# Kernel optimization log

Measured on AMD Instinct MI355X. Metric: run time of the kernel, lower is better.

## Reference

```python
import jax, jax.numpy as jnp
import numpy as np

B, H, W, C = 4, 64, 64, 256
D = C // 8  # q/k projection dim


def setup_inputs() -> dict:
    key = jax.random.key(0)
    ks = jax.random.split(key, 5)
    scale = lambda fan_in: 1.0 / np.sqrt(fan_in)
    return {
        "x": jax.random.normal(ks[0], (B, H, W, C), dtype=jnp.float32),
        "wq": jax.random.normal(ks[1], (C, D), dtype=jnp.float32) * scale(C),
        "bq": jnp.zeros((D,), dtype=jnp.float32),
        "wk": jax.random.normal(ks[2], (C, D), dtype=jnp.float32) * scale(C),
        "bk": jnp.zeros((D,), dtype=jnp.float32),
        "wv": jax.random.normal(ks[3], (C, C), dtype=jnp.float32) * scale(C),
        "bv": jnp.zeros((C,), dtype=jnp.float32),
        "wo": jax.random.normal(ks[4], (C, C), dtype=jnp.float32) * scale(C),
        "bo": jnp.zeros((C,), dtype=jnp.float32),
    }


def reference(x, wq, bq, wk, bk, wv, bv, wo, bo):
    b, h, w, c = x.shape
    n = h * w
    xt = x.reshape(b, n, c)  # 1x1 conv == per-pixel linear over channels
    q = xt @ wq + bq                      # [b, n, d]
    k = xt @ wk + bk                      # [b, n, d]
    v = xt @ wv + bv                      # [b, n, c]
    scores = jnp.einsum("bnd,bmd->bnm", q, k) / jnp.sqrt(jnp.float32(k.shape[-1]))
    attn = jax.nn.softmax(scores, axis=-1)  # [b, n, n]
    attended = jnp.einsum("bnm,bmc->bnc", attn, v)  # [b, n, c]
    out = attended @ wo + bo
    return x + out.reshape(b, h, w, c)
```

## Files before the change

### kernel.cpp

```cpp
#include <hip/hip_runtime.h>
#include <math.h>

#define B_   4
#define N_   4096
#define C_   256
#define D_   32

typedef __attribute__((ext_vector_type(8))) short short8;
typedef __attribute__((ext_vector_type(4))) float f32x4;
typedef __attribute__((ext_vector_type(4))) unsigned short us4;

__device__ __forceinline__ unsigned short f2bf(float f) {
    unsigned int u = __float_as_uint(f);
    u = (u + 0x7FFFu + ((u >> 16) & 1u)) >> 16;
    return (unsigned short)u;
}
__device__ __forceinline__ unsigned short p2bf(float f) {
    return (unsigned short)((__float_as_uint(f) + 0x8000u) >> 16);
}
__device__ __forceinline__ float bf2f(unsigned short h) {
    return __uint_as_float(((unsigned int)h) << 16);
}

__device__ __forceinline__ void dma16(const unsigned short* g, unsigned short* l) {
    __builtin_amdgcn_global_load_lds(
        (const __attribute__((address_space(1))) unsigned int*)(uintptr_t)(g),
        (__attribute__((address_space(3))) unsigned int*)(unsigned int)(uintptr_t)(l),
        16, 0, 0);
}

__global__ __launch_bounds__(256) void prep_w_kernel(const float* __restrict__ wq,
                                                     const float* __restrict__ wk,
                                                     const float* __restrict__ wv,
                                                     const float* __restrict__ wo,
                                                     unsigned short* __restrict__ wqkvT,
                                                     unsigned short* __restrict__ woT) {
    int idx = blockIdx.x * 256 + threadIdx.x;
    if (idx < 320 * 256) {
        int n = idx >> 8, c = idx & 255;
        float v = (n < 32) ? wq[c * 32 + n]
                : (n < 64) ? wk[c * 32 + (n - 32)]
                           : wv[c * 256 + (n - 64)];
        wqkvT[idx] = f2bf(v);
    } else {
        int j = idx - 320 * 256;
        int n = j >> 8, c = j & 255;
        woT[j] = f2bf(wo[c * 256 + n]);
    }
}

__global__ __launch_bounds__(256) void qkv_gemm_kernel(const float* __restrict__ x,
        const unsigned short* __restrict__ wqkvT,
        const float* __restrict__ bq, const float* __restrict__ bk, const float* __restrict__ bv,
        unsigned short* __restrict__ qb, unsigned short* __restrict__ kb,
        unsigned short* __restrict__ vT) {
    const int tid = threadIdx.x;
    const int wave = tid >> 6, lane = tid & 63;
    const int quad = lane >> 4, li = lane & 15;
    const int rows0 = blockIdx.x * 32;
    const float kS = 0.17677669529663687f * 1.4426950408889634f;

    __shared__ __align__(16) unsigned short xs[32 * 264];

#pragma unroll
    for (int i = 0; i < 8; ++i) {
        int flat = i * 256 + tid;
        int row = flat >> 6, c4 = flat & 63;
        float4 f = *(const float4*)(x + (size_t)(rows0 + row) * 256 + c4 * 4);
        us4 o = { f2bf(f.x), f2bf(f.y), f2bf(f.z), f2bf(f.w) };
        *(us4*)&xs[row * 264 + c4 * 4] = o;
    }
    __syncthreads();

    const int rowt = wave & 1;
    const int nt0 = (wave >> 1) * 10;
    const int r0 = rows0 + rowt * 16;

    short8 A[8];
#pragma unroll
    for (int kc = 0; kc < 8; ++kc)
        A[kc] = *(const short8*)&xs[(rowt * 16 + li) * 264 + kc * 32 + quad * 8];

#pragma unroll
    for (int j = 0; j < 10; ++j) {
        const int nt = nt0 + j;
        f32x4 acc = {0.f, 0.f, 0.f, 0.f};
#pragma unroll
        for (int kc = 0; kc < 8; ++kc) {
            short8 Bf = *(const short8*)(wqkvT + (size_t)(nt * 16 + li) * 256 + kc * 32 + quad * 8);
            acc = __builtin_amdgcn_mfma_f32_16x16x32_bf16(A[kc], Bf, acc, 0, 0, 0);
        }
        int n = nt * 16 + li;
        float bias = (nt < 2) ? bq[n] : (nt < 4) ? bk[n - 32] : bv[n - 64];
        if (nt < 4) {
            unsigned short* dst = (nt < 2) ? qb : kb;
            float scl = (nt < 2) ? kS : 1.0f;
            int d = (nt < 2) ? n : (n - 32);
#pragma unroll
            for (int jj = 0; jj < 4; ++jj)
                dst[(size_t)(r0 + quad * 4 + jj) * 32 + d] = f2bf((acc[jj] + bias) * scl);
        } else {
            int c = n - 64;
            int p = r0 + quad * 4;
            int b = p >> 12, ni = p & 4095;
            us4 hv = { f2bf(acc[0] + bias), f2bf(acc[1] + bias),
                       f2bf(acc[2] + bias), f2bf(acc[3] + bias) };
            *(us4*)(vT + ((size_t)(b * 256 + c) * 4096 + ni)) = hv;
        }
    }
}

__global__ __launch_bounds__(256, 2) void attn_partial_kernel(
        const unsigned short* __restrict__ qb, const unsigned short* __restrict__ kb,
        const unsigned short* __restrict__ vT,
        unsigned short* __restrict__ Obf, float* __restrict__ ml) {
    const int tid = threadIdx.x;
    const int wave = tid >> 6, lane = tid & 63;
    const int quad = lane >> 4, li = lane & 15;
    const int by = blockIdx.y, sg = blockIdx.z;
    const int pw = blockIdx.x * 128 + wave * 32;
    const int key0 = sg * 1024;

    __shared__ __align__(16) unsigned short smem[21504];
    unsigned short* v0 = smem;
    unsigned short* v1 = smem + 8192;
    unsigned short* pw_ = smem + 16384 + wave * 1280;

    short8 a_q[2];
#pragma unroll
    for (int qf = 0; qf < 2; ++qf)
        a_q[qf] = *(const short8*)(qb + (size_t)(by * N_ + pw + qf * 16 + li) * 32 + quad * 8);

    const int o8 = lane >> 3, s8 = lane & 7;
    const int sp = s8 ^ o8;
    const int chl = sp >> 2, chk = sp & 3;
    auto stage = [&](int kt, unsigned short* buf) {
#pragma unroll
        for (int h = 0; h < 4; ++h) {
            int ch = ((h * 32 + wave * 8 + o8) << 1) + chl;
            const unsigned short* g = vT + (size_t)(by * 256 + ch) * 4096
                                        + key0 + kt * 32 + chk * 8;
            dma16(g, buf + (h * 256 + wave * 64) * 8);
        }
    };

    stage(0, v0);

    const f32x4 Z = {0.f, 0.f, 0.f, 0.f};
    f32x4 O[2][16];
#pragma unroll
    for (int qf = 0; qf < 2; ++qf)
#pragma unroll
        for (int ct = 0; ct < 16; ++ct) O[qf][ct] = Z;
    f32x4 lsum[2] = {Z, Z};
    short8 ones;
#pragma unroll
    for (int j = 0; j < 8; ++j) ones[j] = (short)0x3F80;

    short8 kf0, kf1;
    {
        const unsigned short* krow = kb + (size_t)(by * N_ + key0) * 32;
        kf0 = *(const short8*)(krow + li * 32 + quad * 8);
        kf1 = *(const short8*)(krow + (16 + li) * 32 + quad * 8);
    }

    const int voff = (li >> 1) * 64 + ((((li & 1) * 4 + quad) ^ ((li >> 1) & 7)) * 8);

    unsigned short* vc = v0;
    unsigned short* vn = v1;
#pragma unroll 1
    for (int kt = 0; kt < 32; ++kt) {
        __builtin_amdgcn_s_waitcnt(0x0f70);
        __syncthreads();

        short8 kn0 = kf0, kn1 = kf1;
        if (kt < 31) {
            stage(kt + 1, vn);
            const unsigned short* krow = kb + (size_t)(by * N_ + key0 + (kt + 1) * 32) * 32;
            kn0 = *(const short8*)(krow + li * 32 + quad * 8);
            kn1 = *(const short8*)(krow + (16 + li) * 32 + quad * 8);
        }

#pragma unroll
        for (int qf = 0; qf < 2; ++qf) {
            f32x4 s0 = __builtin_amdgcn_mfma_f32_16x16x32_bf16(a_q[qf], kf0, Z, 0, 0, 0);
            f32x4 s1 = __builtin_amdgcn_mfma_f32_16x16x32_bf16(a_q[qf], kf1, Z, 0, 0, 0);
#pragma unroll
            for (int r = 0; r < 4; ++r) {
                float p0 = __builtin_amdgcn_exp2f(s0[r]);
                float p1 = __builtin_amdgcn_exp2f(s1[r]);
                pw_[(qf * 16 + quad * 4 + r) * 40 + li]      = p2bf(p0);
                pw_[(qf * 16 + quad * 4 + r) * 40 + 16 + li] = p2bf(p1);
            }
        }

        short8 ap0 = *(const short8*)(pw_ + li * 40 + quad * 8);
        short8 ap1 = *(const short8*)(pw_ + (16 + li) * 40 + quad * 8);
        lsum[0] = __builtin_amdgcn_mfma_f32_16x16x32_bf16(ap0, ones, lsum[0], 0, 0, 0);
        lsum[1] = __builtin_amdgcn_mfma_f32_16x16x32_bf16(ap1, ones, lsum[1], 0, 0, 0);
#pragma unroll
        for (int ct = 0; ct < 16; ++ct) {
            short8 bv8 = *(const short8*)(vc + ct * 512 + voff);
            O[0][ct] = __builtin_amdgcn_mfma_f32_16x16x32_bf16(ap0, bv8, O[0][ct], 0, 0, 0);
            O[1][ct] = __builtin_amdgcn_mfma_f32_16x16x32_bf16(ap1, bv8, O[1][ct], 0, 0, 0);
        }

        kf0 = kn0; kf1 = kn1;
        unsigned short* t = vc; vc = vn; vn = t;
    }

    __syncthreads();
    unsigned short* att = smem + wave * 4224;
    const int srow = lane & 15, scc = (lane >> 4) * 64;
#pragma unroll
    for (int qf = 0; qf < 2; ++qf) {
#pragma unroll
        for (int ct = 0; ct < 16; ++ct)
#pragma unroll
            for (int r = 0; r < 4; ++r)
                att[(quad * 4 + r) * 264 + ct * 16 + li] = f2bf(O[qf][ct][r]);
        const int pbase = by * N_ + pw + qf * 16;
        unsigned short* dst = Obf + ((size_t)(pbase + srow) * 4 + sg) * 256 + scc;
#pragma unroll
        for (int h = 0; h < 8; ++h)
            *(short8*)(dst + h * 8) = *(const short8*)(att + srow * 264 + scc + h * 8);
        if (li == 0) {
#pragma unroll
            for (int r = 0; r < 4; ++r) {
                int pp = pbase + quad * 4 + r;
                ml[pp * 4 + sg] = lsum[qf][r];
            }
        }
    }
}

__global__ __launch_bounds__(256) void merge_proj_kernel(
        const unsigned short* __restrict__ Obf, const float* __restrict__ ml,
        const unsigned short* __restrict__ woT, const float* __restrict__ x,
        const float* __restrict__ bo, float* __restrict__ out) {
    const int tid = threadIdx.x;
    const int px = blockIdx.x * 16;
    __shared__ __align__(16) unsigned short att[16 * 264];

    {
        const int row = tid >> 4, chc = tid & 15;
        const int p = px + row;
        float lt = ml[p * 4] + ml[p * 4 + 1] + ml[p * 4 + 2] + ml[p * 4 + 3];
        float inv = 1.0f / lt;
        float acc[16];
#pragma unroll
        for (int i = 0; i < 16; ++i) acc[i] = 0.f;
#pragma unroll
        for (int s = 0; s < 4; ++s) {
            const unsigned short* src = Obf + (size_t)(p * 4 + s) * 256 + chc * 16;
            short8 v0 = *(const short8*)(src);
            short8 v1 = *(const short8*)(src + 8);
#pragma unroll
            for (int jj = 0; jj < 8; ++jj) {
                acc[jj]     += bf2f((unsigned short)v0[jj]);
                acc[8 + jj] += bf2f((unsigned short)v1[jj]);
            }
        }
        short8 o0, o1;
#pragma unroll
        for (int jj = 0; jj < 8; ++jj) {
            o0[jj] = (short)f2bf(acc[jj] * inv);
            o1[jj] = (short)f2bf(acc[8 + jj] * inv);
        }
        *(short8*)&att[row * 264 + chc * 16]     = o0;
        *(short8*)&att[row * 264 + chc * 16 + 8] = o1;
    }
    __syncthreads();

    const int wave = tid >> 6, lane = tid & 63;
    const int quad = lane >> 4, li = lane & 15;
    short8 bfr[8];
#pragma unroll
    for (int kc = 0; kc < 8; ++kc)
        bfr[kc] = *(const short8*)&att[li * 264 + kc * 32 + quad * 8];
#pragma unroll
    for (int mt = 0; mt < 4; ++mt) {
        const int mtg = wave * 4 + mt;
        f32x4 acc = {0.f, 0.f, 0.f, 0.f};
#pragma unroll
        for (int kc = 0; kc < 8; ++kc) {
            short8 aw = *(const short8*)(woT + (size_t)(mtg * 16 + li) * 256 + kc * 32 + quad * 8);
            acc = __builtin_amdgcn_mfma_f32_16x16x32_bf16(aw, bfr[kc], acc, 0, 0, 0);
        }
        const int pg = px + li;
        const float4 xv  = *(const float4*)(x  + (size_t)pg * 256 + mtg * 16 + quad * 4);
        const float4 bv4 = *(const float4*)(bo + mtg * 16 + quad * 4);
        float4 o4;
        o4.x = acc[0] + xv.x + bv4.x;
        o4.y = acc[1] + xv.y + bv4.y;
        o4.z = acc[2] + xv.z + bv4.z;
        o4.w = acc[3] + xv.w + bv4.w;
        *(float4*)(out + (size_t)pg * 256 + mtg * 16 + quad * 4) = o4;
    }
}

extern "C" void kernel_launch(void* const* d_in, const int* in_sizes, int n_in,
                              void* d_out, int out_size, void* d_ws, size_t ws_size,
                              hipStream_t stream) {
    const float* x  = (const float*)d_in[0];
    const float* wq = (const float*)d_in[1];
    const float* bq = (const float*)d_in[2];
    const float* wk = (const float*)d_in[3];
    const float* bk = (const float*)d_in[4];
    const float* wv = (const float*)d_in[5];
    const float* bv = (const float*)d_in[6];
    const float* wo = (const float*)d_in[7];
    const float* bo = (const float*)d_in[8];
    float* out = (float*)d_out;

    char* ws = (char*)d_ws;
    unsigned short* wqkvT = (unsigned short*)(ws);
    unsigned short* woT   = (unsigned short*)(ws +   163840);
    unsigned short* qb    = (unsigned short*)(ws +   294912);
    unsigned short* kb    = (unsigned short*)(ws +  1343488);
    unsigned short* vT    = (unsigned short*)(ws +  2392064);
    unsigned short* Obf   = (unsigned short*)(ws + 10780672);
    float*          ml    = (float*)         (ws + 44335104);

    hipLaunchKernelGGL(prep_w_kernel,      dim3(576),       dim3(256), 0, stream, wq, wk, wv, wo, wqkvT, woT);
    hipLaunchKernelGGL(qkv_gemm_kernel,    dim3(512),       dim3(256), 0, stream, x, wqkvT, bq, bk, bv, qb, kb, vT);
    hipLaunchKernelGGL(attn_partial_kernel,dim3(32, 4, 4),  dim3(256), 0, stream, qb, kb, vT, Obf, ml);
    hipLaunchKernelGGL(merge_proj_kernel,  dim3(1024),      dim3(256), 0, stream, Obf, ml, woT, x, bo, out);
}
```

Measured before the change: 177.5 us.

## Restructure attention partial kernel to transposed score tiles with register-resident P

The attention inner loop now computes transposed score tiles (K·Q^T), so the exponentiated probabilities land directly in the register layout needed as the B operand of a 16x16x16 bf16 MFMA. This removes the per-iteration LDS round-trip for P. Row sums are now accumulated in scalar registers and reduced with shuffles instead of an extra MFMA against a ones vector. Work is retiled so each wave handles 64 queries by 128 channels with 64-key steps, which doubles the V staging buffer and halves the loop trip count. The cost is higher register pressure, a larger shared-memory footprint that may reduce occupancy, and a different swizzled layout for the output write.

Measured after the change: 262.3 us. 1.48x slower.

```diff
diff --git a/kernel.cpp b/kernel.cpp
--- a/kernel.cpp
+++ b/kernel.cpp
@@ -7,16 +7,16 @@
 #define D_   32
 
 typedef __attribute__((ext_vector_type(8))) short short8;
+typedef __attribute__((ext_vector_type(4))) short short4v;
 typedef __attribute__((ext_vector_type(4))) float f32x4;
 typedef __attribute__((ext_vector_type(4))) unsigned short us4;
+typedef __attribute__((ext_vector_type(2))) int i32x2;
+typedef __attribute__((ext_vector_type(4))) int i32x4;
 
 __device__ __forceinline__ unsigned short f2bf(float f) {
     unsigned int u = __float_as_uint(f);
     u = (u + 0x7FFFu + ((u >> 16) & 1u)) >> 16;
     return (unsigned short)u;
-}
-__device__ __forceinline__ unsigned short p2bf(float f) {
-    return (unsigned short)((__float_as_uint(f) + 0x8000u) >> 16);
 }
 __device__ __forceinline__ float bf2f(unsigned short h) {
     return __uint_as_float(((unsigned int)h) << 16);
@@ -28,6 +28,13 @@
         (__attribute__((address_space(3))) unsigned int*)(unsigned int)(uintptr_t)(l),
         16, 0, 0);
 }
+
+#if __has_builtin(__builtin_amdgcn_mfma_f32_16x16x16bf16_1k)
+#define MFMA16(acc, a, b) acc = __builtin_amdgcn_mfma_f32_16x16x16bf16_1k(a, b, acc, 0, 0, 0)
+#else
+#define MFMA16(acc, a, b) \
+    asm("s_nop 1\n\tv_mfma_f32_16x16x16_bf16 %0, %1, %2, %0" : "+v"(acc) : "v"(a), "v"(b))
+#endif
 
 __global__ __launch_bounds__(256) void prep_w_kernel(const float* __restrict__ wq,
                                                      const float* __restrict__ wk,
@@ -117,120 +124,136 @@
     const int tid = threadIdx.x;
     const int wave = tid >> 6, lane = tid & 63;
     const int quad = lane >> 4, li = lane & 15;
-    const int by = blockIdx.y, sg = blockIdx.z;
-    const int pw = blockIdx.x * 128 + wave * 32;
-    const int key0 = sg * 1024;
-
-    __shared__ __align__(16) unsigned short smem[21504];
+    const int by = blockIdx.y, seg = blockIdx.z;
+    const int qh = wave >> 1, chh = wave & 1;
+    const int qw = blockIdx.x * 128 + qh * 64;
+    const int key0 = seg * 1024;
+
+    __shared__ __align__(16) unsigned short smem[32768];
     unsigned short* v0 = smem;
-    unsigned short* v1 = smem + 8192;
-    unsigned short* pw_ = smem + 16384 + wave * 1280;
-
-    short8 a_q[2];
-#pragma unroll
-    for (int qf = 0; qf < 2; ++qf)
-        a_q[qf] = *(const short8*)(qb + (size_t)(by * N_ + pw + qf * 16 + li) * 32 + quad * 8);
-
-    const int o8 = lane >> 3, s8 = lane & 7;
-    const int sp = s8 ^ o8;
-    const int chl = sp >> 2, chk = sp & 3;
+    unsigned short* v1 = smem + 16384;
+
+    short8 a_q[4];
+#pragma unroll
+    for (int qf = 0; qf < 4; ++qf)
+        a_q[qf] = *(const short8*)(qb + (size_t)(by * N_ + qw + qf * 16 + li) * 32 + quad * 8);
+
+    const int sch = tid >> 3;
+    const int sgi = (tid & 7) ^ (sch & 7);
+    const unsigned short* vsrc0 = vT + (size_t)(by * 256 + sch) * 4096 + key0 + sgi * 8;
+    const int ldss = wave * 512;
     auto stage = [&](int kt, unsigned short* buf) {
 #pragma unroll
-        for (int h = 0; h < 4; ++h) {
-            int ch = ((h * 32 + wave * 8 + o8) << 1) + chl;
-            const unsigned short* g = vT + (size_t)(by * 256 + ch) * 4096
-                                        + key0 + kt * 32 + chk * 8;
-            dma16(g, buf + (h * 256 + wave * 64) * 8);
-        }
+        for (int h = 0; h < 8; ++h)
+            dma16(vsrc0 + kt * 64 + (size_t)h * 32 * 4096, buf + h * 2048 + ldss);
     };
-
     stage(0, v0);
 
     const f32x4 Z = {0.f, 0.f, 0.f, 0.f};
-    f32x4 O[2][16];
-#pragma unroll
-    for (int qf = 0; qf < 2; ++qf)
-#pragma unroll
-        for (int ct = 0; ct < 16; ++ct) O[qf][ct] = Z;
-    f32x4 lsum[2] = {Z, Z};
-    short8 ones;
-#pragma unroll
-    for (int j = 0; j < 8; ++j) ones[j] = (short)0x3F80;
-
-    short8 kf0, kf1;
-    {
-        const unsigned short* krow = kb + (size_t)(by * N_ + key0) * 32;
-        kf0 = *(const short8*)(krow + li * 32 + quad * 8);
-        kf1 = *(const short8*)(krow + (16 + li) * 32 + quad * 8);
-    }
-
-    const int voff = (li >> 1) * 64 + ((((li & 1) * 4 + quad) ^ ((li >> 1) & 7)) * 8);
+    f32x4 acc[8][4];
+#pragma unroll
+    for (int ct = 0; ct < 8; ++ct)
+#pragma unroll
+        for (int qf = 0; qf < 4; ++qf) acc[ct][qf] = Z;
+    float ps[4] = {0.f, 0.f, 0.f, 0.f};
+
+    short8 kf[4];
+#pragma unroll
+    for (int kk = 0; kk < 4; ++kk)
+        kf[kk] = *(const short8*)(kb + (size_t)(by * N_ + key0 + kk * 16 + li) * 32 + quad * 8);
+
+    const int w0 = (quad >> 1) ^ (li & 7);
+    const int vbl = (chh * 128 + li) * 64 + (quad & 1) * 4;
 
     unsigned short* vc = v0;
     unsigned short* vn = v1;
 #pragma unroll 1
-    for (int kt = 0; kt < 32; ++kt) {
+    for (int kt = 0; kt < 16; ++kt) {
         __builtin_amdgcn_s_waitcnt(0x0f70);
         __syncthreads();
 
-        short8 kn0 = kf0, kn1 = kf1;
-        if (kt < 31) {
+        short8 kn[4];
+        if (kt < 15) {
             stage(kt + 1, vn);
-            const unsigned short* krow = kb + (size_t)(by * N_ + key0 + (kt + 1) * 32) * 32;
-            kn0 = *(const short8*)(krow + li * 32 + quad * 8);
-            kn1 = *(const short8*)(krow + (16 + li) * 32 + quad * 8);
-        }
-
-#pragma unroll
-        for (int qf = 0; qf < 2; ++qf) {
-            f32x4 s0 = __builtin_amdgcn_mfma_f32_16x16x32_bf16(a_q[qf], kf0, Z, 0, 0, 0);
-            f32x4 s1 = __builtin_amdgcn_mfma_f32_16x16x32_bf16(a_q[qf], kf1, Z, 0, 0, 0);
-#pragma unroll
-            for (int r = 0; r < 4; ++r) {
-                float p0 = __builtin_amdgcn_exp2f(s0[r]);
-                float p1 = __builtin_amdgcn_exp2f(s1[r]);
-                pw_[(qf * 16 + quad * 4 + r) * 40 + li]      = p2bf(p0);
-                pw_[(qf * 16 + quad * 4 + r) * 40 + 16 + li] = p2bf(p1);
+            const unsigned short* krow = kb + (size_t)(by * N_ + key0 + (kt + 1) * 64) * 32;
+#pragma unroll
+            for (int kk = 0; kk < 4; ++kk)
+                kn[kk] = *(const short8*)(krow + (kk * 16 + li) * 32 + quad * 8);
+        } else {
+#pragma unroll
+            for (int kk = 0; kk < 4; ++kk) kn[kk] = kf[kk];
+        }
+
+#pragma unroll
+        for (int kk = 0; kk < 4; ++kk) {
+            short4v pb[4];
+#pragma unroll
+            for (int qf = 0; qf < 4; ++qf) {
+                f32x4 st = __builtin_amdgcn_mfma_f32_16x16x32_bf16(kf[kk], a_q[qf], Z, 0, 0, 0);
+                float p0 = __builtin_amdgcn_exp2f(st[0]);
+                float p1 = __builtin_amdgcn_exp2f(st[1]);
+                float p2 = __builtin_amdgcn_exp2f(st[2]);
+                float p3 = __builtin_amdgcn_exp2f(st[3]);
+                ps[qf] += (p0 + p1) + (p2 + p3);
+                unsigned u0 = __float_as_uint(p0) + 0x8000u;
+                unsigned u1 = __float_as_uint(p1) + 0x8000u;
+                unsigned u2 = __float_as_uint(p2) + 0x8000u;
+                unsigned u3 = __float_as_uint(p3) + 0x8000u;
+                i32x2 t;
+                t[0] = (int)((u0 >> 16) | (u1 & 0xFFFF0000u));
+                t[1] = (int)((u2 >> 16) | (u3 & 0xFFFF0000u));
+                pb[qf] = __builtin_bit_cast(short4v, t);
             }
-        }
-
-        short8 ap0 = *(const short8*)(pw_ + li * 40 + quad * 8);
-        short8 ap1 = *(const short8*)(pw_ + (16 + li) * 40 + quad * 8);
-        lsum[0] = __builtin_amdgcn_mfma_f32_16x16x32_bf16(ap0, ones, lsum[0], 0, 0, 0);
-        lsum[1] = __builtin_amdgcn_mfma_f32_16x16x32_bf16(ap1, ones, lsum[1], 0, 0, 0);
-#pragma unroll
-        for (int ct = 0; ct < 16; ++ct) {
-            short8 bv8 = *(const short8*)(vc + ct * 512 + voff);
-            O[0][ct] = __builtin_amdgcn_mfma_f32_16x16x32_bf16(ap0, bv8, O[0][ct], 0, 0, 0);
-            O[1][ct] = __builtin_amdgcn_mfma_f32_16x16x32_bf16(ap1, bv8, O[1][ct], 0, 0, 0);
-        }
-
-        kf0 = kn0; kf1 = kn1;
+            const int go = ((kk * 2) ^ w0) * 8;
+#pragma unroll
+            for (int ct = 0; ct < 8; ++ct) {
+                short4v av = *(const short4v*)(vc + vbl + ct * 1024 + go);
+                MFMA16(acc[ct][0], av, pb[0]);
+                MFMA16(acc[ct][1], av, pb[1]);
+                MFMA16(acc[ct][2], av, pb[2]);
+                MFMA16(acc[ct][3], av, pb[3]);
+            }
+        }
+#pragma unroll
+        for (int kk = 0; kk < 4; ++kk) kf[kk] = kn[kk];
         unsigned short* t = vc; vc = vn; vn = t;
     }
 
     __syncthreads();
-    unsigned short* att = smem + wave * 4224;
-    const int srow = lane & 15, scc = (lane >> 4) * 64;
-#pragma unroll
-    for (int qf = 0; qf < 2; ++qf) {
-#pragma unroll
-        for (int ct = 0; ct < 16; ++ct)
-#pragma unroll
-            for (int r = 0; r < 4; ++r)
-                att[(quad * 4 + r) * 264 + ct * 16 + li] = f2bf(O[qf][ct][r]);
-        const int pbase = by * N_ + pw + qf * 16;
-        unsigned short* dst = Obf + ((size_t)(pbase + srow) * 4 + sg) * 256 + scc;
-#pragma unroll
-        for (int h = 0; h < 8; ++h)
-            *(short8*)(dst + h * 8) = *(const short8*)(att + srow * 264 + scc + h * 8);
-        if (li == 0) {
-#pragma unroll
-            for (int r = 0; r < 4; ++r) {
-                int pp = pbase + quad * 4 + r;
-                ml[pp * 4 + sg] = lsum[qf][r];
-            }
-        }
+    asm volatile("s_nop 7\n\ts_nop 7" :: );
+
+#pragma unroll
+    for (int qf = 0; qf < 4; ++qf) {
+        float l = ps[qf];
+        l += __shfl_xor(l, 16);
+        l += __shfl_xor(l, 32);
+        if (chh == 0 && quad == 0)
+            ml[(size_t)(by * N_ + qw + qf * 16 + li) * 4 + seg] = l;
+    }
+
+    unsigned short* att = smem;
+#pragma unroll
+    for (int ct = 0; ct < 8; ++ct)
+#pragma unroll
+        for (int qf = 0; qf < 4; ++qf) {
+            int q = qh * 64 + qf * 16 + li;
+            int g = chh * 16 + ct * 2 + (quad >> 1);
+            int addr = q * 256 + ((g ^ (li & 7)) * 8) + (quad & 1) * 4;
+            us4 hv = { f2bf(acc[ct][qf][0]), f2bf(acc[ct][qf][1]),
+                       f2bf(acc[ct][qf][2]), f2bf(acc[ct][qf][3]) };
+            *(us4*)(att + addr) = hv;
+        }
+    __syncthreads();
+
+    const int rq = tid >> 1, hf = tid & 1;
+    const int p = blockIdx.x * 128 + rq;
+    unsigned short* dst = Obf + ((size_t)(by * N_ + p) * 4 + seg) * 256 + hf * 128;
+    const int sw7 = rq & 7;
+#pragma unroll
+    for (int gg = 0; gg < 16; ++gg) {
+        int g = hf * 16 + gg;
+        i32x4 val = *(const i32x4*)(att + rq * 256 + ((g ^ sw7) * 8));
+        *(i32x4*)(dst + gg * 8) = val;
     }
 }
 
```
